# Kernel tuning notes

Hardware: AMD Instinct MI355X
Metric: run time of the kernel (lower is better)

## Reference

```python
import jax, jax.numpy as jnp
import numpy as np

K = 32                      # nsample (neighbors)
NPTS = [4096, 2048, 1024]   # npts // downsample_ratios [1,2,4]
CH = [(6, 64, 64), (134, 128, 128), (262, 256, 256)]  # (c_in_edge, c_mid, c_out) per EdgeConv
OUT_CH = 128
EPS = 1e-5


def setup_inputs():
    key = jax.random.key(0)
    ks = iter(jax.random.split(key, 64))
    d = {"pcd": jax.random.normal(next(ks), (8, 4096, 3), dtype=jnp.float32)}
    for li, (cin, cmid, cout) in enumerate(CH, start=1):
        d[f"W{li}a"] = jax.random.normal(next(ks), (cmid, cin), dtype=jnp.float32) * 0.05
        d[f"b{li}a"] = jax.random.normal(next(ks), (cmid,), dtype=jnp.float32) * 0.01
        d[f"g{li}a"] = jnp.ones((cmid,), dtype=jnp.float32)
        d[f"be{li}a"] = jnp.zeros((cmid,), dtype=jnp.float32)
        d[f"W{li}b"] = jax.random.normal(next(ks), (cout, cmid), dtype=jnp.float32) * 0.05
        d[f"b{li}b"] = jax.random.normal(next(ks), (cout,), dtype=jnp.float32) * 0.01
        d[f"g{li}b"] = jnp.ones((cout,), dtype=jnp.float32)
        d[f"be{li}b"] = jnp.zeros((cout,), dtype=jnp.float32)
    d["fcW"] = jax.random.normal(next(ks), (OUT_CH, CH[-1][2]), dtype=jnp.float32) * 0.05
    d["fcb"] = jnp.zeros((OUT_CH,), dtype=jnp.float32)
    return d


def _knn_idx(q, p, k):
    # q: [B,m,3] queries, p: [B,n,3] points -> [B,m,k] nearest-neighbor indices
    d = (jnp.sum(q * q, -1)[:, :, None] + jnp.sum(p * p, -1)[:, None, :]
         - 2.0 * jnp.einsum('bmd,bnd->bmn', q, p))
    _, idx = jax.lax.top_k(-d, k)
    return idx


def _bn(x, g, b):
    # training-mode BatchNorm2d over [B,C,m,k], biased variance (torch behavior)
    mu = jnp.mean(x, axis=(0, 2, 3), keepdims=True)
    var = jnp.mean((x - mu) ** 2, axis=(0, 2, 3), keepdims=True)
    return (x - mu) * jax.lax.rsqrt(var + EPS) * g[None, :, None, None] + b[None, :, None, None]


def _edge_conv(xyz, feat, npoints, params):
    # xyz: [B,n,3], feat: [B,C,n] or None. Range sampling = first npoints points.
    W1, b1, g1, be1, W2, b2, g2, be2 = params
    new_xyz = xyz[:, :npoints]
    # use_xyz=True: concat features (as [B,n,C]) with xyz
    f = xyz if feat is None else jnp.concatenate([jnp.transpose(feat, (0, 2, 1)), xyz], -1)
    new_f = f[:, :npoints]                       # [B,m,D]
    idx = _knn_idx(new_xyz, xyz, K)              # [B,m,K]
    knn_f = jax.vmap(lambda a, i: a[i])(f, idx)  # [B,m,K,D] gather
    tiled = jnp.broadcast_to(new_f[:, :, None, :], knn_f.shape)
    e = jnp.concatenate([knn_f - tiled, tiled], -1)  # [B,m,K,2D] edge features
    h = jnp.einsum('bmkc,oc->bomk', e, W1) + b1[None, :, None, None]
    h = jax.nn.relu(_bn(h, g1, be1))
    h = jnp.einsum('bcmk,oc->bomk', h, W2) + b2[None, :, None, None]
    h = jax.nn.relu(_bn(h, g2, be2))
    return new_xyz, jnp.max(h, axis=-1)          # max-pool over K -> [B,C,m]


def reference(pcd, W1a, b1a, g1a, be1a, W1b, b1b, g1b, be1b,
              W2a, b2a, g2a, be2a, W2b, b2b, g2b, be2b,
              W3a, b3a, g3a, be3a, W3b, b3b, g3b, be3b, fcW, fcb):
    xyz = pcd[..., :3]
    feat = None  # pcd has only xyz channels
    layer_params = [
        (W1a, b1a, g1a, be1a, W1b, b1b, g1b, be1b),
        (W2a, b2a, g2a, be2a, W2b, b2b, g2b, be2b),
        (W3a, b3a, g3a, be3a, W3b, b3b, g3b, be3b),
    ]
    for npoints, p in zip(NPTS, layer_params):
        xyz, feat = _edge_conv(xyz, feat, npoints, p)
    out_feat = jnp.einsum('bcn,oc->bon', feat, fcW) + fcb[None, :, None]
    # Range sampling: idx chain of aranges composes to arange(NPTS[-1])
    idx = jnp.broadcast_to(jnp.arange(NPTS[-1]), (pcd.shape[0], NPTS[-1]))
    return xyz, out_feat, idx, feat
```

## Files before the change

kernel.cpp:

```cpp
#include <hip/hip_runtime.h>
#include <hip/hip_bf16.h>

#define B8 8
#define KNN 32
typedef unsigned short u16;
typedef unsigned int u32;
typedef unsigned long long u64;

typedef __attribute__((ext_vector_type(8))) _Float16 half8;
typedef __attribute__((ext_vector_type(4))) float f32x4;

static __device__ __forceinline__ u16 f2h_u(float f) {
  _Float16 h = (_Float16)f; u16 u; __builtin_memcpy(&u, &h, 2); return u;
}

static __device__ __forceinline__ u64 enc_key(float d, int id) {
  u32 u = __float_as_uint(d);
  u = (d >= 0.f) ? (u | 0x80000000u) : ~u;
  return ((u64)u << 32) | (u32)id;
}
static __device__ __forceinline__ float dec_val(u64 k) {
  u32 u = (u32)(k >> 32);
  u = (u & 0x80000000u) ? (u & 0x7fffffffu) : ~u;
  return __uint_as_float(u);
}

static __device__ __forceinline__ u64 rank64(u64 mk, int lane, u64* slk, u64* outk, float& tau) {
  slk[lane] = mk;
  int r = 0;
#pragma unroll 16
  for (int j = 0; j < 64; ++j) r += (slk[j] < mk) ? 1 : 0;
  outk[r] = mk;
  u64 res = outk[lane];
  tau = dec_val(outk[31]);
  return res;
}

__global__ __launch_bounds__(256) void knn_kernel(const float* __restrict__ pcd,
                                                  int N, int M, int* __restrict__ idxout) {
  __shared__ float4 pts[1024];
  __shared__ u64 bufk[4][32];
  __shared__ u64 slk[4][64];
  __shared__ u64 outk[4][64];
  const int t = threadIdx.x;
  const int lane = t & 63, w = t >> 6;
  const int b = blockIdx.y;
  const int m = blockIdx.x * 4 + w;
  const float* base = pcd + (size_t)b * 4096 * 3;
  const float qx = base[m*3], qy = base[m*3+1], qz = base[m*3+2];
  const float ax = -2.f*qx, ay = -2.f*qy, az = -2.f*qz;

  u64 heldk;
  float tau;
  int cnt = 0;

  for (int i = t; i < 1024; i += 256) {
    const float* p = base + (size_t)i * 3;
    float x = p[0], y = p[1], z = p[2];
    pts[i] = make_float4(x, y, z, x*x + y*y + z*z);
  }
  __syncthreads();

  {
    float4 p = pts[lane];
    float r0 = fmaf(ax, p.x, fmaf(ay, p.y, fmaf(az, p.z, p.w)));
    heldk = rank64(enc_key(r0, lane), lane, slk[w], outk[w], tau);
  }

  for (int n0 = 0; n0 < N; n0 += 1024) {
    if (n0) {
      __syncthreads();
      for (int i = t; i < 1024; i += 256) {
        const float* p = base + (size_t)(n0 + i) * 3;
        float x = p[0], y = p[1], z = p[2];
        pts[i] = make_float4(x, y, z, x*x + y*y + z*z);
      }
      __syncthreads();
    }
    for (int c = 0; c < 1024; c += 256) {
      float4 p0 = pts[c + lane];
      float4 p1 = pts[c + 64 + lane];
      float4 p2 = pts[c + 128 + lane];
      float4 p3 = pts[c + 192 + lane];
      float r[4];
      r[0] = fmaf(ax, p0.x, fmaf(ay, p0.y, fmaf(az, p0.z, p0.w)));
      r[1] = fmaf(ax, p1.x, fmaf(ay, p1.y, fmaf(az, p1.z, p1.w)));
      r[2] = fmaf(ax, p2.x, fmaf(ay, p2.y, fmaf(az, p2.z, p2.w)));
      r[3] = fmaf(ax, p3.x, fmaf(ay, p3.y, fmaf(az, p3.z, p3.w)));
      if (n0 == 0 && c == 0) r[0] = 3.4e38f;
      float rmn = fminf(fminf(r[0], r[1]), fminf(r[2], r[3]));
      if (!__any(rmn < tau)) continue;
#pragma unroll
      for (int j = 0; j < 4; ++j) {
        float rr = r[j];
        if (!__any(rr < tau)) continue;
        int gid = n0 + c + j * 64 + lane;
        bool pass = rr < tau;
        while (__any(pass)) {
          u64 mk_ = __ballot(pass);
          int before = __popcll(mk_ & ((1ull << lane) - 1ull));
          int total  = __popcll(mk_);
          int room = 32 - cnt;
          if (pass && before < room) {
            bufk[w][cnt + before] = enc_key(rr, gid);
            pass = false;
          }
          if (total >= room) {
            u64 mk = (lane < 32) ? heldk : bufk[w][lane - 32];
            heldk = rank64(mk, lane, slk[w], outk[w], tau);
            cnt = 0;
            pass = pass && (rr < tau);
          } else {
            cnt += total;
          }
        }
      }
    }
  }
  if (cnt > 0) {
    int bl = lane - 32;
    u64 mk = (lane < 32) ? heldk
             : ((bl < cnt) ? bufk[w][bl]
                           : ((0xFFFFFFFFull << 32) | (0xFFFFFF00u | (u32)lane)));
    heldk = rank64(mk, lane, slk[w], outk[w], tau);
  }
  if (lane < KNN) idxout[((size_t)b * M + m) * KNN + lane] = (int)(u32)(heldk & 0xFFFFFFFFu);
}

__global__ void prep_all(
    const float* __restrict__ W1a, const float* __restrict__ W1b,
    const float* __restrict__ W2a, const float* __restrict__ W2b,
    const float* __restrict__ W3a, const float* __restrict__ W3b,
    float* __restrict__ RED,
    float* __restrict__ WAT1, float* __restrict__ WBT1, u16* __restrict__ WBH1,
    float* __restrict__ WBT2, u16* __restrict__ WAH2, u16* __restrict__ WBH2,
    float* __restrict__ WBT3, u16* __restrict__ WAH3, u16* __restrict__ WBH3)
{
  int i0 = blockIdx.x * 256 + threadIdx.x;
  int NT = gridDim.x * 256;
  for (int i = i0; i < 8192; i += NT) RED[i] = 0.f;
  for (int i = i0; i < 256; i += NT) {
    int c = i >> 6, o = i & 63;
    float w1 = (c < 3) ? W1a[o*6 + c] : 0.f;
    float w2 = (c < 3) ? W1a[o*6 + 3 + c] : 0.f;
    WAT1[i] = w1; WBT1[i] = w2 - w1;
  }
  for (int i = i0; i < 4096; i += NT) WBH1[i] = f2h_u(W1b[i]);
  for (int i = i0; i < 68*128; i += NT) {
    int c = i >> 7, o = i & 127;
    float w1 = 0.f, w2 = 0.f;
    if (c < 67) { w1 = W2a[o*134 + c]; w2 = W2a[o*134 + 67 + c]; }
    WBT2[i] = w2 - w1;
  }
  for (int i = i0; i < 128*128; i += NT) {
    int o = i >> 7, k = i & 127;
    WAH2[i] = (k < 67) ? f2h_u(W2a[o*134 + k]) : (u16)0;
  }
  for (int i = i0; i < 16384; i += NT) WBH2[i] = f2h_u(W2b[i]);
  for (int i = i0; i < 132*256; i += NT) {
    int c = i >> 8, o = i & 255;
    float w1 = 0.f, w2 = 0.f;
    if (c < 131) { w1 = W3a[o*262 + c]; w2 = W3a[o*262 + 131 + c]; }
    WBT3[i] = w2 - w1;
  }
  for (int i = i0; i < 256*192; i += NT) {
    int o = i / 192, k = i - o * 192;
    WAH3[i] = (k < 131) ? f2h_u(W3a[o*262 + k]) : (u16)0;
  }
  for (int i = i0; i < 65536; i += NT) WBH3[i] = f2h_u(W3b[i]);
}

template<int C2, int CM, int MODE>
__global__ __launch_bounds__(256) void conv_a_gemm(
    const float* __restrict__ F, size_t fbstride,
    const int* __restrict__ idx,
    const float* __restrict__ Wt,
    const float* __restrict__ bias,
    const float* __restrict__ T,
    float* __restrict__ Tout,
    float* __restrict__ red_s, float* __restrict__ red_q,
    int M)
{
  constexpr int KP = (C2 + 3) & ~3;
  constexpr int KC = (KP <= 68) ? KP : 44;
  __shared__ float At[64][KC];
  __shared__ float Wts[KC][64];
  __shared__ int ji[64];
  __shared__ float sred[4][64];
  __shared__ float qred[4][64];
  const int t = threadIdx.x;
  const int rt = blockIdx.x, ot = blockIdx.y, b = blockIdx.z;
  const int R0 = rt * 64, oc0 = ot * 64;
  const float* Fb = F + (size_t)b * fbstride;

  if (t < 64) {
    int gr = R0 + t;
    ji[t] = (MODE == 0) ? gr : idx[((size_t)b * M + (gr >> 5)) * KNN + (gr & 31)];
  }

  const int cg = t & 15, rg = t >> 4;
  const int r0 = rg * 4, c0 = cg * 4;
  float acc[4][4];
  if (MODE == 0) {
#pragma unroll
    for (int j = 0; j < 4; ++j) {
      float bv = bias[oc0 + c0 + j];
#pragma unroll
      for (int i = 0; i < 4; ++i) acc[i][j] = bv;
    }
  } else {
#pragma unroll
    for (int i = 0; i < 4; ++i) {
      const float* tp = T + ((size_t)b * M + (size_t)((R0 + r0 + i) >> 5)) * CM + oc0 + c0;
      acc[i][0] = tp[0]; acc[i][1] = tp[1]; acc[i][2] = tp[2]; acc[i][3] = tp[3];
    }
  }
  __syncthreads();

  for (int k0 = 0; k0 < KP; k0 += KC) {
    if (k0) __syncthreads();
    for (int i = t; i < KC * 64; i += 256) {
      int c = i >> 6, o = i & 63;
      Wts[c][o] = Wt[(size_t)(k0 + c) * CM + oc0 + o];
    }
    if constexpr (C2 == 3) {
      for (int i = t; i < 64 * 4; i += 256) {
        int r = i >> 2, c = i & 3;
        At[r][c] = (c < 3) ? Fb[(size_t)ji[r] * 3 + c] : 0.f;
      }
    } else {
      constexpr int C4 = KC / 4;
      for (int i = t; i < 64 * C4; i += 256) {
        int r = i / C4, c4 = i - r * C4;
        *(float4*)&At[r][c4 * 4] = *(const float4*)&Fb[(size_t)ji[r] * KP + k0 + c4 * 4];
      }
    }
    __syncthreads();

#pragma unroll 4
    for (int k = 0; k < KC; ++k) {
      const float4 w4 = *(const float4*)&Wts[k][c0];
      float a0 = At[r0][k], a1 = At[r0+1][k], a2 = At[r0+2][k], a3 = At[r0+3][k];
      acc[0][0]=fmaf(a0,w4.x,acc[0][0]); acc[0][1]=fmaf(a0,w4.y,acc[0][1]);
      acc[0][2]=fmaf(a0,w4.z,acc[0][2]); acc[0][3]=fmaf(a0,w4.w,acc[0][3]);
      acc[1][0]=fmaf(a1,w4.x,acc[1][0]); acc[1][1]=fmaf(a1,w4.y,acc[1][1]);
      acc[1][2]=fmaf(a1,w4.z,acc[1][2]); acc[1][3]=fmaf(a1,w4.w,acc[1][3]);
      acc[2][0]=fmaf(a2,w4.x,acc[2][0]); acc[2][1]=fmaf(a2,w4.y,acc[2][1]);
      acc[2][2]=fmaf(a2,w4.z,acc[2][2]); acc[2][3]=fmaf(a2,w4.w,acc[2][3]);
      acc[3][0]=fmaf(a3,w4.x,acc[3][0]); acc[3][1]=fmaf(a3,w4.y,acc[3][1]);
      acc[3][2]=fmaf(a3,w4.z,acc[3][2]); acc[3][3]=fmaf(a3,w4.w,acc[3][3]);
    }
  }

  if (MODE == 0) {
    float* op = Tout + ((size_t)b * M + R0) * (size_t)CM + oc0;
#pragma unroll
    for (int i = 0; i < 4; ++i) {
      float* p = op + (size_t)(r0 + i) * CM + c0;
      p[0]=acc[i][0]; p[1]=acc[i][1]; p[2]=acc[i][2]; p[3]=acc[i][3];
    }
  } else {
    float cs[4], cq_[4];
#pragma unroll
    for (int j = 0; j < 4; ++j) {
      float s = acc[0][j] + acc[1][j] + acc[2][j] + acc[3][j];
      float q = acc[0][j]*acc[0][j] + acc[1][j]*acc[1][j] + acc[2][j]*acc[2][j] + acc[3][j]*acc[3][j];
      s += __shfl_xor(s, 16); q += __shfl_xor(q, 16);
      s += __shfl_xor(s, 32); q += __shfl_xor(q, 32);
      cs[j] = s; cq_[j] = q;
    }
    const int wv = t >> 6;
    if ((t & 48) == 0) {
#pragma unroll
      for (int j = 0; j < 4; ++j) { sred[wv][c0 + j] = cs[j]; qred[wv][c0 + j] = cq_[j]; }
    }
    __syncthreads();
    if (t < 64) {
      float s = sred[0][t] + sred[1][t] + sred[2][t] + sred[3][t];
      float q = qred[0][t] + qred[1][t] + qred[2][t] + qred[3][t];
      int shdw = (rt & 15) * 256;
      atomicAdd(&red_s[shdw + t], s);
      atomicAdd(&red_q[shdw + t], q);
    }
  }
}

__global__ __launch_bounds__(256) void l1_convb(
    const float* __restrict__ pcd,
    const int* __restrict__ idx,
    const float* __restrict__ WAT,
    const float* __restrict__ T,
    const u16* __restrict__ Wbh,
    const float* __restrict__ bb,
    const float* __restrict__ sc1, const float* __restrict__ sh1,
    float* __restrict__ red_s, float* __restrict__ red_q,
    float* __restrict__ hmax)
{
  __shared__ u16 Alds[64][72];
  __shared__ u16 Wlds[64][72];
  __shared__ float xyzs[64][4];
  __shared__ float was[3][64];
  __shared__ float scs[64], shs[64];
  __shared__ int ji[64];
  const int t = threadIdx.x;
  const int lane = t & 63, w = t >> 6;
  const int wr = w >> 1, wc = w & 1;
  const int cl = lane & 15, rq = lane >> 4;
  const int rt = blockIdx.x, b = blockIdx.y;
  const int R0 = rt * 64;
  const float* pb = pcd + (size_t)b * 12288;

  if (t < 64) ji[t] = idx[((size_t)b * 4096 + ((R0 + t) >> 5)) * KNN + ((R0 + t) & 31)];
  if (t < 192) was[t / 64][t & 63] = WAT[t];
  if (t >= 192) { int c = t - 192; scs[c] = sc1[c]; shs[c] = sh1[c]; }
  if (t >= 192) {  }
  for (int i = t; i < 64 * 8; i += 256) {
    int o = i >> 3, seg = i & 7;
    *(float4*)&Wlds[o][seg * 8] = *(const float4*)&Wbh[(size_t)o * 64 + seg * 8];
  }
  __syncthreads();
  if (t < 64) {
    const float* p = pb + (size_t)ji[t] * 3;
    xyzs[t][0] = p[0]; xyzs[t][1] = p[1]; xyzs[t][2] = p[2]; xyzs[t][3] = 0.f;
  }
  if (t < 64) { scs[t] = sc1[t]; shs[t] = sh1[t]; }
  __syncthreads();

  for (int i = t; i < 64 * 8; i += 256) {
    int r = i >> 3, seg = i & 7;
    float px = xyzs[r][0], py = xyzs[r][1], pz = xyzs[r][2];
    const float* Tm = T + ((size_t)b * 4096 + (size_t)((R0 + r) >> 5)) * 64;
    half8 ov;
#pragma unroll
    for (int j2 = 0; j2 < 8; ++j2) {
      int c = seg * 8 + j2;
      float h = Tm[c];
      h = fmaf(px, was[0][c], h);
      h = fmaf(py, was[1][c], h);
      h = fmaf(pz, was[2][c], h);
      ov[j2] = (_Float16)fmaxf(0.f, fmaf(h, scs[c], shs[c]));
    }
    *(half8*)&Alds[r][seg * 8] = ov;
  }
  __syncthreads();

  f32x4 acc[2][2];
#pragma unroll
  for (int fr = 0; fr < 2; ++fr)
#pragma unroll
    for (int fc = 0; fc < 2; ++fc) {
      float bv = bb[wc * 32 + fc * 16 + cl];
#pragma unroll
      for (int r = 0; r < 4; ++r) acc[fr][fc][r] = bv;
    }

#pragma unroll
  for (int kk = 0; kk < 2; ++kk) {
    half8 af[2], bf[2];
#pragma unroll
    for (int fr = 0; fr < 2; ++fr)
      af[fr] = *(const half8*)&Alds[wr*32 + fr*16 + cl][kk*32 + rq*8];
#pragma unroll
    for (int fc = 0; fc < 2; ++fc)
      bf[fc] = *(const half8*)&Wlds[wc*32 + fc*16 + cl][kk*32 + rq*8];
#pragma unroll
    for (int fr = 0; fr < 2; ++fr)
#pragma unroll
      for (int fc = 0; fc < 2; ++fc)
        acc[fr][fc] = __builtin_amdgcn_mfma_f32_16x16x32_f16(af[fr], bf[fc], acc[fr][fc], 0, 0, 0);
  }

#pragma unroll
  for (int fc = 0; fc < 2; ++fc) {
    float s = 0.f, q = 0.f, mx = -3.4e38f;
#pragma unroll
    for (int fr = 0; fr < 2; ++fr)
#pragma unroll
      for (int r = 0; r < 4; ++r) {
        float v = acc[fr][fc][r];
        s += v; q += v * v; mx = fmaxf(mx, v);
      }
    s += __shfl_xor(s, 16); q += __shfl_xor(q, 16); mx = fmaxf(mx, __shfl_xor(mx, 16));
    s += __shfl_xor(s, 32); q += __shfl_xor(q, 32); mx = fmaxf(mx, __shfl_xor(mx, 32));
    if (rq == 0) {
      int col = wc * 32 + fc * 16 + cl;
      int shdw = (rt & 15) * 256;
      atomicAdd(&red_s[shdw + col], s);
      atomicAdd(&red_q[shdw + col], q);
      hmax[((size_t)b * 4096 + (size_t)(rt * 2 + wr)) * 64 + col] = mx;
    }
  }
}

template<int CM, int KPAD>
__global__ __launch_bounds__(256) void conv_a_mfma(
    const float* __restrict__ F, int fstride, size_t fbstride,
    const int* __restrict__ idx,
    const u16* __restrict__ Wh,
    const float* __restrict__ T,
    u16* __restrict__ Hout,
    float* __restrict__ red_s, float* __restrict__ red_q,
    int M)
{
  constexpr int FC = CM / 32;
  __shared__ u16 Alds[64][72];
  __shared__ u16 Wlds[CM][72];
  __shared__ int ji[64];
  const int t = threadIdx.x;
  const int lane = t & 63, w = t >> 6;
  const int wr = w >> 1, wc = w & 1;
  const int cl = lane & 15, rq = lane >> 4;
  const int rt = blockIdx.x, b = blockIdx.y;
  const int R0 = rt * 64;
  const float* Fb = F + (size_t)b * fbstride;

  if (t < 64) ji[t] = idx[((size_t)b * M + ((R0 + t) >> 5)) * KNN + ((R0 + t) & 31)];

  f32x4 acc[2][FC];
#pragma unroll
  for (int fr = 0; fr < 2; ++fr)
#pragma unroll
    for (int fc = 0; fc < FC; ++fc) {
      int col = wc * (CM/2) + fc * 16 + cl;
#pragma unroll
      for (int r = 0; r < 4; ++r) {
        int row = R0 + wr*32 + fr*16 + rq*4 + r;
        acc[fr][fc][r] = T[((size_t)b * M + (row >> 5)) * CM + col];
      }
    }
  __syncthreads();

  for (int k0 = 0; k0 < KPAD; k0 += 64) {
    if (k0) __syncthreads();
    for (int i = t; i < 64 * 16; i += 256) {
      int r = i >> 4, seg = i & 15;
      int k = k0 + seg * 4;
      ushort4 s = {0,0,0,0};
      if (k < fstride) {
        float4 v = *(const float4*)&Fb[(size_t)ji[r] * fstride + k];
        s.x = f2h_u(v.x); s.y = f2h_u(v.y); s.z = f2h_u(v.z); s.w = f2h_u(v.w);
      }
      *(ushort4*)&Alds[r][seg * 4] = s;
    }
    for (int i = t; i < CM * 8; i += 256) {
      int o = i >> 3, seg = i & 7;
      *(float4*)&Wlds[o][seg * 8] = *(const float4*)&Wh[(size_t)o * KPAD + k0 + seg * 8];
    }
    __syncthreads();

#pragma unroll
    for (int kk = 0; kk < 2; ++kk) {
      half8 af[2], bf[FC];
#pragma unroll
      for (int fr = 0; fr < 2; ++fr)
        af[fr] = *(const half8*)&Alds[wr*32 + fr*16 + cl][kk*32 + rq*8];
#pragma unroll
      for (int fc = 0; fc < FC; ++fc)
        bf[fc] = *(const half8*)&Wlds[wc*(CM/2) + fc*16 + cl][kk*32 + rq*8];
#pragma unroll
      for (int fr = 0; fr < 2; ++fr)
#pragma unroll
        for (int fc = 0; fc < FC; ++fc)
          acc[fr][fc] = __builtin_amdgcn_mfma_f32_16x16x32_f16(af[fr], bf[fc], acc[fr][fc], 0, 0, 0);
    }
  }

  u16* Hb = Hout + ((size_t)b * (size_t)M * KNN + R0) * CM;
#pragma unroll
  for (int fr = 0; fr < 2; ++fr)
#pragma unroll
    for (int fc = 0; fc < FC; ++fc) {
      int col = wc*(CM/2) + fc*16 + cl;
#pragma unroll
      for (int r = 0; r < 4; ++r) {
        int row = wr*32 + fr*16 + rq*4 + r;
        Hb[(size_t)row * CM + col] = f2h_u(acc[fr][fc][r]);
      }
    }

#pragma unroll
  for (int fc = 0; fc < FC; ++fc) {
    float s = 0.f, q = 0.f;
#pragma unroll
    for (int fr = 0; fr < 2; ++fr)
#pragma unroll
      for (int r = 0; r < 4; ++r) {
        float v = acc[fr][fc][r];
        s += v; q += v * v;
      }
    s += __shfl_xor(s, 16); q += __shfl_xor(q, 16);
    s += __shfl_xor(s, 32); q += __shfl_xor(q, 32);
    if (rq == 0) {
      int col = wc*(CM/2) + fc*16 + cl;
      int shdw = (rt & 15) * 256;
      atomicAdd(&red_s[shdw + col], s);
      atomicAdd(&red_q[shdw + col], q);
    }
  }
}

template<int CM>
__global__ __launch_bounds__(256) void conv_b_fused(
    const u16* __restrict__ H,
    const u16* __restrict__ Wh,
    const float* __restrict__ bb,
    const float* __restrict__ sc1, const float* __restrict__ sh1,
    float* __restrict__ red_s, float* __restrict__ red_q,
    float* __restrict__ hmax,
    int Mrows)
{
  constexpr int FC = CM / 32;
  __shared__ u16 Alds[64][72];
  __shared__ u16 Wlds[CM][72];
  __shared__ float scs[CM], shs[CM];
  const int t = threadIdx.x;
  const int lane = t & 63, w = t >> 6;
  const int wr = w >> 1, wc = w & 1;
  const int cl = lane & 15, rq = lane >> 4;
  const int rt = blockIdx.x, b = blockIdx.y;
  const u16* Hb = H + ((size_t)b * Mrows + (size_t)rt * 64) * CM;

  for (int i = t; i < CM; i += 256) { scs[i] = sc1[i]; shs[i] = sh1[i]; }

  f32x4 acc[2][FC];
#pragma unroll
  for (int fr = 0; fr < 2; ++fr)
#pragma unroll
    for (int fc = 0; fc < FC; ++fc) {
      float bv = bb[wc * (CM/2) + fc * 16 + cl];
#pragma unroll
      for (int r = 0; r < 4; ++r) acc[fr][fc][r] = bv;
    }
  __syncthreads();

  for (int k0 = 0; k0 < CM; k0 += 64) {
    if (k0) __syncthreads();
    for (int i = t; i < 64 * 8; i += 256) {
      int r = i >> 3, seg = i & 7;
      half8 hv = *(const half8*)&Hb[(size_t)r * CM + k0 + seg * 8];
      half8 ov;
#pragma unroll
      for (int j = 0; j < 8; ++j) {
        int c = k0 + seg * 8 + j;
        float v = fmaxf(0.f, fmaf((float)hv[j], scs[c], shs[c]));
        ov[j] = (_Float16)v;
      }
      *(half8*)&Alds[r][seg * 8] = ov;
    }
    for (int i = t; i < CM * 8; i += 256) {
      int o = i >> 3, seg = i & 7;
      *(float4*)&Wlds[o][seg * 8] = *(const float4*)&Wh[(size_t)o * CM + k0 + seg * 8];
    }
    __syncthreads();

#pragma unroll
    for (int kk = 0; kk < 2; ++kk) {
      half8 af[2], bf[FC];
#pragma unroll
      for (int fr = 0; fr < 2; ++fr)
        af[fr] = *(const half8*)&Alds[wr*32 + fr*16 + cl][kk*32 + rq*8];
#pragma unroll
      for (int fc = 0; fc < FC; ++fc)
        bf[fc] = *(const half8*)&Wlds[wc*(CM/2) + fc*16 + cl][kk*32 + rq*8];
#pragma unroll
      for (int fr = 0; fr < 2; ++fr)
#pragma unroll
        for (int fc = 0; fc < FC; ++fc)
          acc[fr][fc] = __builtin_amdgcn_mfma_f32_16x16x32_f16(af[fr], bf[fc], acc[fr][fc], 0, 0, 0);
    }
  }

#pragma unroll
  for (int fc = 0; fc < FC; ++fc) {
    float s = 0.f, q = 0.f, mx = -3.4e38f;
#pragma unroll
    for (int fr = 0; fr < 2; ++fr)
#pragma unroll
      for (int r = 0; r < 4; ++r) {
        float v = acc[fr][fc][r];
        s += v; q += v * v; mx = fmaxf(mx, v);
      }
    s += __shfl_xor(s, 16); q += __shfl_xor(q, 16); mx = fmaxf(mx, __shfl_xor(mx, 16));
    s += __shfl_xor(s, 32); q += __shfl_xor(q, 32); mx = fmaxf(mx, __shfl_xor(mx, 32));
    if (rq == 0) {
      int col = wc*(CM/2) + fc*16 + cl;
      int shdw = (rt & 15) * 256;
      atomicAdd(&red_s[shdw + col], s);
      atomicAdd(&red_q[shdw + col], q);
      hmax[((size_t)b * (Mrows >> 5) + (size_t)(rt * 2 + wr)) * CM + col] = mx;
    }
  }
}

__global__ void bn_finalize(float* __restrict__ red_s, float* __restrict__ red_q,
                            const float* __restrict__ g, const float* __restrict__ be,
                            float* __restrict__ sc, float* __restrict__ sh,
                            int cm, float invcnt) {
  int o = threadIdx.x;
  if (o < cm) {
    float s = 0.f, q = 0.f;
    for (int i = 0; i < 16; ++i) { s += red_s[i * 256 + o]; q += red_q[i * 256 + o]; }
    float mu  = s * invcnt;
    float var = fmaxf(q * invcnt - mu * mu, 0.f);
    float scv = g[o] * rsqrtf(var + 1e-5f);
    sc[o] = scv;
    sh[o] = fmaf(-mu, scv, be[o]);
  }
  __syncthreads();
  for (int i = threadIdx.x; i < 16 * 256; i += 256) { red_s[i] = 0.f; red_q[i] = 0.f; }
}

__global__ __launch_bounds__(256) void bnrelu_fb(const float* __restrict__ hm,
    const float* __restrict__ sc2, const float* __restrict__ sh2,
    float* __restrict__ fout, int CM, int fostride, size_t fobstride, int M) {
  int i = blockIdx.x * 256 + threadIdx.x;
  int cq = CM >> 2;
  int total = B8 * M * cq;
  if (i >= total) return;
  int c4 = i % cq; int r = i / cq;
  int b = r / M, m = r - b * M;
  float4 v = *(const float4*)&hm[((size_t)b * M + m) * CM + c4 * 4];
  int c = c4 * 4;
  float4 o;
  o.x = fmaxf(0.f, fmaf(v.x, sc2[c],   sh2[c]));
  o.y = fmaxf(0.f, fmaf(v.y, sc2[c+1], sh2[c+1]));
  o.z = fmaxf(0.f, fmaf(v.z, sc2[c+2], sh2[c+2]));
  o.w = fmaxf(0.f, fmaf(v.w, sc2[c+3], sh2[c+3]));
  *(float4*)&fout[(size_t)b * fobstride + (size_t)m * fostride + c] = o;
}

__global__ void append_xyz(const float* __restrict__ pcd, float* __restrict__ fbuf,
                           int nrows, int stride, int coff) {
  int i = blockIdx.x * 256 + threadIdx.x;
  if (i < B8 * nrows) {
    int b = i / nrows, n = i - b * nrows;
    const float* p = pcd + ((size_t)b * 4096 + n) * 3;
    float* dd = fbuf + ((size_t)b * nrows + n) * stride + coff;
    dd[0] = p[0]; dd[1] = p[1]; dd[2] = p[2]; dd[3] = 0.f;
  }
}

__global__ __launch_bounds__(256) void fc_out(const float* __restrict__ f4,
                                              const float* __restrict__ fcW, const float* __restrict__ fcb,
                                              float* __restrict__ out1, float* __restrict__ out3) {
  __shared__ float tile[32 * 257];
  const int t = threadIdx.x, b = blockIdx.x, n0 = blockIdx.y * 32;
  for (int i = t; i < 32 * 256; i += 256) {
    int n = i >> 8, c = i & 255;
    tile[n * 257 + c] = f4[((size_t)b * 1024 + n0 + n) * 256 + c];
  }
  __syncthreads();
  const int n = t & 31, og = t >> 5;
#pragma unroll
  for (int ci = 0; ci < 32; ++ci) {
    int c = og * 32 + ci;
    out3[((size_t)b * 256 + c) * 1024 + n0 + n] = tile[n * 257 + c];
  }
#pragma unroll
  for (int oi = 0; oi < 16; ++oi) {
    int o = og * 16 + oi;
    float acc = fcb[o];
    const float* w = fcW + (size_t)o * 256;
#pragma unroll 4
    for (int c = 0; c < 256; ++c) acc = fmaf(tile[n * 257 + c], w[c], acc);
    out1[((size_t)b * 128 + o) * 1024 + n0 + n] = acc;
  }
}

__global__ void out_xyz_idx(const float* __restrict__ pcd, float* __restrict__ out0,
                            float* __restrict__ out2) {
  int i = blockIdx.x * 256 + threadIdx.x;
  if (i < B8 * 1024) {
    int b = i >> 10, n = i & 1023;
    const float* p = pcd + ((size_t)b * 4096 + n) * 3;
    float* o = out0 + (size_t)i * 3;
    o[0] = p[0]; o[1] = p[1]; o[2] = p[2];
    out2[i] = (float)n;
  }
}

extern "C" void kernel_launch(void* const* d_in, const int* in_sizes, int n_in,
                              void* d_out, int out_size, void* d_ws, size_t ws_size,
                              hipStream_t stream) {
  (void)in_sizes; (void)n_in; (void)out_size; (void)ws_size;
  const float* pcd = (const float*)d_in[0];
  const float* W1a = (const float*)d_in[1];  const float* b1a = (const float*)d_in[2];
  const float* g1a = (const float*)d_in[3];  const float* be1a= (const float*)d_in[4];
  const float* W1b = (const float*)d_in[5];  const float* b1b = (const float*)d_in[6];
  const float* g1b = (const float*)d_in[7];  const float* be1b= (const float*)d_in[8];
  const float* W2a = (const float*)d_in[9];  const float* b2a = (const float*)d_in[10];
  const float* g2a = (const float*)d_in[11]; const float* be2a= (const float*)d_in[12];
  const float* W2b = (const float*)d_in[13]; const float* b2b = (const float*)d_in[14];
  const float* g2b = (const float*)d_in[15]; const float* be2b= (const float*)d_in[16];
  const float* W3a = (const float*)d_in[17]; const float* b3a = (const float*)d_in[18];
  const float* g3a = (const float*)d_in[19]; const float* be3a= (const float*)d_in[20];
  const float* W3b = (const float*)d_in[21]; const float* b3b = (const float*)d_in[22];
  const float* g3b = (const float*)d_in[23]; const float* be3b= (const float*)d_in[24];
  const float* fcW = (const float*)d_in[25]; const float* fcb = (const float*)d_in[26];

  float* wsf = (float*)d_ws;
  float* FB2 = wsf;
  float* FB3 = FB2 + 2228224;
  float* FB4 = FB3 + 2162688;
  float* TBUF= FB4 + 2097152;
  float* RED = TBUF + 2097152;
  float* red_s = RED, *red_q = RED + 4096;
  float* SC1 = RED + 8192;  float* SH1 = SC1 + 256;
  float* SC2 = SH1 + 256;   float* SH2 = SC2 + 256;
  float* WAT1 = SH2 + 256;
  float* WBT1 = WAT1 + 256;
  float* WBT2 = WBT1 + 256;
  float* WBT3 = WBT2 + 8704;
  float* HMAX = WBT3 + 33792;
  int* IDX1 = (int*)(HMAX + 2097152);
  int* IDX2 = IDX1 + (size_t)8 * 4096 * 32;
  int* IDX3 = IDX2 + (size_t)8 * 2048 * 32;
  u16* H    = (u16*)(IDX3 + (size_t)8 * 1024 * 32);
  u16* WBH1 = H + (size_t)67108864;
  u16* WAH2 = WBH1 + 4096;
  u16* WBH2 = WAH2 + 16384;
  u16* WAH3 = WBH2 + 16384;
  u16* WBH3 = WAH3 + 49152;

  float* out0 = (float*)d_out;
  float* out1 = out0 + 24576;
  float* out2 = out1 + 1048576;
  float* out3 = out2 + 8192;

  prep_all<<<64, 256, 0, stream>>>(W1a, W1b, W2a, W2b, W3a, W3b, RED,
                                   WAT1, WBT1, WBH1, WBT2, WAH2, WBH2, WBT3, WAH3, WBH3);

  knn_kernel<<<dim3(1024, 8), 256, 0, stream>>>(pcd, 4096, 4096, IDX1);
  conv_a_gemm<3,64,0><<<dim3(64,1,8),256,0,stream>>>(pcd,(size_t)12288,nullptr,WBT1,b1a,nullptr,TBUF,nullptr,nullptr,4096);
  conv_a_gemm<3,64,1><<<dim3(2048,1,8),256,0,stream>>>(pcd,(size_t)12288,IDX1,WAT1,nullptr,TBUF,nullptr,red_s,red_q,4096);
  bn_finalize<<<1,256,0,stream>>>(red_s,red_q,g1a,be1a,SC1,SH1,64,1.f/1048576.f);
  l1_convb<<<dim3(2048,8),256,0,stream>>>(pcd,IDX1,WAT1,TBUF,WBH1,b1b,SC1,SH1,red_s,red_q,HMAX);
  bn_finalize<<<1,256,0,stream>>>(red_s,red_q,g1b,be1b,SC2,SH2,64,1.f/1048576.f);
  bnrelu_fb<<<2048,256,0,stream>>>(HMAX,SC2,SH2,FB2,64,68,(size_t)278528,4096);
  append_xyz<<<128, 256, 0, stream>>>(pcd, FB2, 4096, 68, 64);

  knn_kernel<<<dim3(512, 8), 256, 0, stream>>>(pcd, 4096, 2048, IDX2);
  conv_a_gemm<67,128,0><<<dim3(32,2,8),256,0,stream>>>(FB2,(size_t)278528,nullptr,WBT2,b2a,nullptr,TBUF,nullptr,nullptr,2048);
  conv_a_mfma<128,128><<<dim3(1024,8),256,0,stream>>>(FB2,68,(size_t)278528,IDX2,WAH2,TBUF,H,red_s,red_q,2048);
  bn_finalize<<<1,256,0,stream>>>(red_s,red_q,g2a,be2a,SC1,SH1,128,1.f/524288.f);
  conv_b_fused<128><<<dim3(1024,8),256,0,stream>>>(H,WBH2,b2b,SC1,SH1,red_s,red_q,HMAX,2048*32);
  bn_finalize<<<1,256,0,stream>>>(red_s,red_q,g2b,be2b,SC2,SH2,128,1.f/524288.f);
  bnrelu_fb<<<2048,256,0,stream>>>(HMAX,SC2,SH2,FB3,128,132,(size_t)270336,2048);
  append_xyz<<<64, 256, 0, stream>>>(pcd, FB3, 2048, 132, 128);

  knn_kernel<<<dim3(256, 8), 256, 0, stream>>>(pcd, 2048, 1024, IDX3);
  conv_a_gemm<131,256,0><<<dim3(16,4,8),256,0,stream>>>(FB3,(size_t)270336,nullptr,WBT3,b3a,nullptr,TBUF,nullptr,nullptr,1024);
  conv_a_mfma<256,192><<<dim3(512,8),256,0,stream>>>(FB3,132,(size_t)270336,IDX3,WAH3,TBUF,H,red_s,red_q,1024);
  bn_finalize<<<1,256,0,stream>>>(red_s,red_q,g3a,be3a,SC1,SH1,256,1.f/262144.f);
  conv_b_fused<256><<<dim3(512,8),256,0,stream>>>(H,WBH3,b3b,SC1,SH1,red_s,red_q,HMAX,1024*32);
  bn_finalize<<<1,256,0,stream>>>(red_s,red_q,g3b,be3b,SC2,SH2,256,1.f/262144.f);
  bnrelu_fb<<<2048,256,0,stream>>>(HMAX,SC2,SH2,FB4,256,256,(size_t)262144,1024);

  fc_out<<<dim3(8, 32), 256, 0, stream>>>(FB4, fcW, fcb, out1, out3);
  out_xyz_idx<<<32, 256, 0, stream>>>(pcd, out0, out2);
}
```

Baseline: 872.7 us.

## Store conv-a intermediate as packed fp8 and widen conv_b blocks to 512 threads

The conv_a_mfma output H is now stored as fp8, with four rows packed per u32 via cvt_pk_fp8, instead of fp16. conv_b_fused unpacks it with cvt_f32_fp8 before applying BN+ReLU, and now runs 512-thread blocks covering 128 rows each. The aim is to halve the traffic of the large intermediate write and read and to give each block more waves. It trades precision, since fp8 carries roughly a 3-bit mantissa on pre-BN activations and may breach tolerance. The unpack path also does scattered per-byte u32 loads that may coalesce poorly.

```diff
diff --git a/kernel.cpp b/kernel.cpp
--- a/kernel.cpp
+++ b/kernel.cpp
@@ -50,9 +50,7 @@
   const float qx = base[m*3], qy = base[m*3+1], qz = base[m*3+2];
   const float ax = -2.f*qx, ay = -2.f*qy, az = -2.f*qz;
 
-  u64 heldk;
-  float tau;
-  int cnt = 0;
+  u64 heldk; float tau; int cnt = 0;
 
   for (int i = t; i < 1024; i += 256) {
     const float* p = base + (size_t)i * 3;
@@ -312,8 +310,6 @@
 
   if (t < 64) ji[t] = idx[((size_t)b * 4096 + ((R0 + t) >> 5)) * KNN + ((R0 + t) & 31)];
   if (t < 192) was[t / 64][t & 63] = WAT[t];
-  if (t >= 192) { int c = t - 192; scs[c] = sc1[c]; shs[c] = sh1[c]; }
-  if (t >= 192) {  }
   for (int i = t; i < 64 * 8; i += 256) {
     int o = i >> 3, seg = i & 7;
     *(float4*)&Wlds[o][seg * 8] = *(const float4*)&Wbh[(size_t)o * 64 + seg * 8];
@@ -398,7 +394,7 @@
     const int* __restrict__ idx,
     const u16* __restrict__ Wh,
     const float* __restrict__ T,
-    u16* __restrict__ Hout,
+    u32* __restrict__ H32,
     float* __restrict__ red_s, float* __restrict__ red_q,
     int M)
 {
@@ -465,17 +461,15 @@
     }
   }
 
-  u16* Hb = Hout + ((size_t)b * (size_t)M * KNN + R0) * CM;
+  u32* Hb4 = H32 + ((size_t)b * ((size_t)M * KNN / 4) + (size_t)(R0 >> 2)) * CM;
 #pragma unroll
   for (int fr = 0; fr < 2; ++fr)
 #pragma unroll
     for (int fc = 0; fc < FC; ++fc) {
       int col = wc*(CM/2) + fc*16 + cl;
-#pragma unroll
-      for (int r = 0; r < 4; ++r) {
-        int row = wr*32 + fr*16 + rq*4 + r;
-        Hb[(size_t)row * CM + col] = f2h_u(acc[fr][fc][r]);
-      }
+      u32 v = __builtin_amdgcn_cvt_pk_fp8_f32(acc[fr][fc][0], acc[fr][fc][1], 0, false);
+      v = __builtin_amdgcn_cvt_pk_fp8_f32(acc[fr][fc][2], acc[fr][fc][3], v, true);
+      Hb4[(size_t)(wr*8 + fr*4 + rq) * CM + col] = v;
     }
 
 #pragma unroll
@@ -500,8 +494,8 @@
 }
 
 template<int CM>
-__global__ __launch_bounds__(256) void conv_b_fused(
-    const u16* __restrict__ H,
+__global__ __launch_bounds__(512) void conv_b_fused(
+    const u32* __restrict__ H32,
     const u16* __restrict__ Wh,
     const float* __restrict__ bb,
     const float* __restrict__ sc1, const float* __restrict__ sh1,
@@ -510,17 +504,18 @@
     int Mrows)
 {
   constexpr int FC = CM / 32;
-  __shared__ u16 Alds[64][72];
+  __shared__ u16 Alds[128][72];
   __shared__ u16 Wlds[CM][72];
   __shared__ float scs[CM], shs[CM];
   const int t = threadIdx.x;
   const int lane = t & 63, w = t >> 6;
-  const int wr = w >> 1, wc = w & 1;
+  const int wr = w >> 1;
+  const int wc = w & 1;
   const int cl = lane & 15, rq = lane >> 4;
   const int rt = blockIdx.x, b = blockIdx.y;
-  const u16* Hb = H + ((size_t)b * Mrows + (size_t)rt * 64) * CM;
-
-  for (int i = t; i < CM; i += 256) { scs[i] = sc1[i]; shs[i] = sh1[i]; }
+  const u32* Hb4 = H32 + ((size_t)b * ((size_t)Mrows / 4) + (size_t)(rt * 32)) * CM;
+
+  for (int i = t; i < CM; i += 512) { scs[i] = sc1[i]; shs[i] = sh1[i]; }
 
   f32x4 acc[2][FC];
 #pragma unroll
@@ -535,19 +530,21 @@
 
   for (int k0 = 0; k0 < CM; k0 += 64) {
     if (k0) __syncthreads();
-    for (int i = t; i < 64 * 8; i += 256) {
+    for (int i = t; i < 128 * 8; i += 512) {
       int r = i >> 3, seg = i & 7;
-      half8 hv = *(const half8*)&Hb[(size_t)r * CM + k0 + seg * 8];
+      int rg = r >> 2, sh8 = (r & 3) * 8;
+      const u32* hp = Hb4 + (size_t)rg * CM + k0 + seg * 8;
       half8 ov;
 #pragma unroll
       for (int j = 0; j < 8; ++j) {
+        float v = __builtin_amdgcn_cvt_f32_fp8((hp[j] >> sh8) & 0xffu, 0);
         int c = k0 + seg * 8 + j;
-        float v = fmaxf(0.f, fmaf((float)hv[j], scs[c], shs[c]));
+        v = fmaxf(0.f, fmaf(v, scs[c], shs[c]));
         ov[j] = (_Float16)v;
       }
       *(half8*)&Alds[r][seg * 8] = ov;
     }
-    for (int i = t; i < CM * 8; i += 256) {
+    for (int i = t; i < CM * 8; i += 512) {
       int o = i >> 3, seg = i & 7;
       *(float4*)&Wlds[o][seg * 8] = *(const float4*)&Wh[(size_t)o * CM + k0 + seg * 8];
     }
@@ -587,7 +584,7 @@
       int shdw = (rt & 15) * 256;
       atomicAdd(&red_s[shdw + col], s);
       atomicAdd(&red_q[shdw + col], q);
-      hmax[((size_t)b * (Mrows >> 5) + (size_t)(rt * 2 + wr)) * CM + col] = mx;
+      hmax[((size_t)b * (Mrows >> 5) + (size_t)(rt * 4 + wr)) * CM + col] = mx;
     }
   }
 }
@@ -715,8 +712,8 @@
   int* IDX1 = (int*)(HMAX + 2097152);
   int* IDX2 = IDX1 + (size_t)8 * 4096 * 32;
   int* IDX3 = IDX2 + (size_t)8 * 2048 * 32;
-  u16* H    = (u16*)(IDX3 + (size_t)8 * 1024 * 32);
-  u16* WBH1 = H + (size_t)67108864;
+  u32* H32  = (u32*)(IDX3 + (size_t)8 * 1024 * 32);
+  u16* WBH1 = (u16*)(H32 + 16777216);
   u16* WAH2 = WBH1 + 4096;
   u16* WBH2 = WAH2 + 16384;
   u16* WAH3 = WBH2 + 16384;
@@ -741,18 +738,18 @@
 
   knn_kernel<<<dim3(512, 8), 256, 0, stream>>>(pcd, 4096, 2048, IDX2);
   conv_a_gemm<67,128,0><<<dim3(32,2,8),256,0,stream>>>(FB2,(size_t)278528,nullptr,WBT2,b2a,nullptr,TBUF,nullptr,nullptr,2048);
-  conv_a_mfma<128,128><<<dim3(1024,8),256,0,stream>>>(FB2,68,(size_t)278528,IDX2,WAH2,TBUF,H,red_s,red_q,2048);
+  conv_a_mfma<128,128><<<dim3(1024,8),256,0,stream>>>(FB2,68,(size_t)278528,IDX2,WAH2,TBUF,H32,red_s,red_q,2048);
   bn_finalize<<<1,256,0,stream>>>(red_s,red_q,g2a,be2a,SC1,SH1,128,1.f/524288.f);
-  conv_b_fused<128><<<dim3(1024,8),256,0,stream>>>(H,WBH2,b2b,SC1,SH1,red_s,red_q,HMAX,2048*32);
+  conv_b_fused<128><<<dim3(512,8),512,0,stream>>>(H32,WBH2,b2b,SC1,SH1,red_s,red_q,HMAX,2048*32);
   bn_finalize<<<1,256,0,stream>>>(red_s,red_q,g2b,be2b,SC2,SH2,128,1.f/524288.f);
   bnrelu_fb<<<2048,256,0,stream>>>(HMAX,SC2,SH2,FB3,128,132,(size_t)270336,2048);
   append_xyz<<<64, 256, 0, stream>>>(pcd, FB3, 2048, 132, 128);
 
   knn_kernel<<<dim3(256, 8), 256, 0, stream>>>(pcd, 2048, 1024, IDX3);
   conv_a_gemm<131,256,0><<<dim3(16,4,8),256,0,stream>>>(FB3,(size_t)270336,nullptr,WBT3,b3a,nullptr,TBUF,nullptr,nullptr,1024);
-  conv_a_mfma<256,192><<<dim3(512,8),256,0,stream>>>(FB3,132,(size_t)270336,IDX3,WAH3,TBUF,H,red_s,red_q,1024);
+  conv_a_mfma<256,192><<<dim3(512,8),256,0,stream>>>(FB3,132,(size_t)270336,IDX3,WAH3,TBUF,H32,red_s,red_q,1024);
   bn_finalize<<<1,256,0,stream>>>(red_s,red_q,g3a,be3a,SC1,SH1,256,1.f/262144.f);
-  conv_b_fused<256><<<dim3(512,8),256,0,stream>>>(H,WBH3,b3b,SC1,SH1,red_s,red_q,HMAX,1024*32);
+  conv_b_fused<256><<<dim3(256,8),512,0,stream>>>(H32,WBH3,b3b,SC1,SH1,red_s,red_q,HMAX,1024*32);
   bn_finalize<<<1,256,0,stream>>>(red_s,red_q,g3b,be3b,SC2,SH2,256,1.f/262144.f);
   bnrelu_fb<<<2048,256,0,stream>>>(HMAX,SC2,SH2,FB4,256,256,(size_t)262144,1024);
 
```

Measured after the change: 849.7 us. -2.6%, faster.
